# Kernel optimization log

Hardware: AMD Instinct MI355X
Metric: run time of the kernel (lower is better)

Reference implementation:

```python
import jax, jax.numpy as jnp
import numpy as np

N = 65536          # number of input vectors
D = 128            # embedding_dim
K = 2048           # num_embeddings (codebook size)
DH = D // 2        # linear_proj output dim


def setup_inputs() -> dict:
    key = jax.random.key(0)
    k1, k2, k3, k4 = jax.random.split(key, 4)
    z = jax.random.normal(k1, (N, D), dtype=jnp.float32)
    # linear_proj params (nn.Linear(D, D//2)): weight [DH, D], bias [DH]
    W = jax.random.normal(k2, (DH, D), dtype=jnp.float32) * (1.0 / np.sqrt(D))
    b = jax.random.normal(k3, (DH,), dtype=jnp.float32) * 0.01
    # codebook buffer, initialized ~ N(0,1) as in the torch module
    embeddings = jax.random.normal(k4, (K, D), dtype=jnp.float32)
    return {"z": z, "W": W, "b": b, "embeddings": embeddings}


def reference(z, W, b, embeddings):
    # project inputs and codebook into half-dim space
    z_ = z @ W.T + b                       # [N, DH]
    emb_ = embeddings @ W.T + b            # [K, DH]
    # squared euclidean distances via ||a||^2 + ||b||^2 - 2 a.b
    distances = ((z_ ** 2).sum(-1, keepdims=True)
                 + (emb_ ** 2).sum(-1)
                 - 2.0 * (z_ @ emb_.T))    # [N, K]
    closest = jnp.argmin(distances, axis=-1)               # [N]
    one_hot_encoding = jax.nn.one_hot(closest, K, dtype=jnp.float32)  # [N, K]
    quantized = one_hot_encoding @ embeddings               # [N, D] (gather)
    return (quantized, one_hot_encoding)
```

## Files before the change

### kernel.cpp

```cpp
#include <hip/hip_runtime.h>
#include <float.h>

#define N_ROWS 65536
#define D_IN   128
#define DH     64
#define K_CB   2048

typedef const __attribute__((address_space(1))) void* gas_p;
typedef __attribute__((address_space(3))) void* las_p;
typedef _Float16 f16x8 __attribute__((ext_vector_type(8)));
typedef float    f32x4 __attribute__((ext_vector_type(4)));

__global__ __launch_bounds__(256) void k_project(
    const float* __restrict__ Z, const float* __restrict__ emb,
    const float* __restrict__ W, const float* __restrict__ b,
    _Float16* __restrict__ zpl,
    _Float16* __restrict__ epl,
    float* __restrict__ e2,
    float* __restrict__ outOH) {
  __shared__ __align__(16) float Wl[64 * 140];
  __shared__ __align__(16) float Zl[16 * 128];
  int tid = threadIdx.x;
  const float* src; _Float16* dst; int n0; bool do_e2; size_t plane;
  if ((int)blockIdx.x < 4096) {
    src = Z;   dst = zpl; n0 = blockIdx.x * 16;          do_e2 = false; plane = (size_t)N_ROWS * 64;
  } else {
    src = emb; dst = epl; n0 = (blockIdx.x - 4096) * 16; do_e2 = true;  plane = (size_t)K_CB * 64;
  }

#pragma unroll
  for (int i = 0; i < 8; ++i) {
    int idx4 = tid + 256 * i;
    int j = idx4 >> 5;
    int d4 = (idx4 & 31) * 4;
    *(float4*)&Wl[j * 140 + d4] = *(const float4*)(W + j * 128 + d4);
  }
#pragma unroll
  for (int i = 0; i < 2; ++i) {
    int idx4 = tid + 256 * i;
    int r = idx4 >> 5;
    int d4 = (idx4 & 31) * 4;
    *(float4*)&Zl[r * 128 + d4] = *(const float4*)(src + (size_t)(n0 + r) * 128 + d4);
  }
  int j = tid & 63, g = tid >> 6;
  float bj = b[j];
  __syncthreads();

  if (outOH && (int)blockIdx.x < 4096) {
    f32x4 zz4 = (f32x4){0.f, 0.f, 0.f, 0.f};
    f32x4* dz = (f32x4*)(outOH + (size_t)n0 * K_CB);
#pragma unroll
    for (int i = 0; i < 32; ++i)
      __builtin_nontemporal_store(zz4, dz + tid + 256 * i);
  }

  float acc[4] = {0.f, 0.f, 0.f, 0.f};
  for (int d4 = 0; d4 < 128; d4 += 4) {
    float4 w4 = *(float4*)&Wl[j * 140 + d4];
#pragma unroll
    for (int i = 0; i < 4; ++i) {
      float4 z4 = *(float4*)&Zl[(g * 4 + i) * 128 + d4];
      acc[i] = fmaf(z4.x, w4.x, fmaf(z4.y, w4.y, fmaf(z4.z, w4.z, fmaf(z4.w, w4.w, acc[i]))));
    }
  }
#pragma unroll
  for (int i = 0; i < 4; ++i) {
    int n = n0 + g * 4 + i;
    float v = acc[i] + bj;
    _Float16 h = (_Float16)v;  float rm = v - (float)h;
    _Float16 m = (_Float16)rm;
    int pos = (((j >> 3) ^ (n & 7)) << 3) | (j & 7);
    size_t base = (size_t)n * 64 + pos;
    dst[base]         = h;
    dst[plane + base] = m;
    if (do_e2) {
      float s = v * v;
#pragma unroll
      for (int off = 32; off > 0; off >>= 1) s += __shfl_xor(s, off, 64);
      if (j == 0) e2[n] = s;
    }
  }
}

__global__ __launch_bounds__(256, 3) void k_score(
    const _Float16* __restrict__ zpl,
    const _Float16* __restrict__ epl,
    const float* __restrict__ e2,
    const float* __restrict__ emb,
    float* __restrict__ outQ,
    float* __restrict__ outOH,
    int* __restrict__ cidx_g) {
  __shared__ __align__(16) _Float16 Zs[2 * 64 * 64];
  __shared__ __align__(16) _Float16 Es[2 * 128 * 64];
  __shared__ float e2s[128];

  int tid = threadIdx.x, lane = tid & 63, wid = tid >> 6;
  int quad = lane >> 4, l16 = lane & 15;
  int wcol = wid * 32;
  int row0 = blockIdx.x * 64;

  for (int q = wid; q < 16; q += 4) {
    int p = q >> 3, within = (q & 7) * 1024;
    const char* g = (const char*)zpl + (size_t)p * ((size_t)N_ROWS * 128)
                  + (size_t)row0 * 128 + within + lane * 16;
    __builtin_amdgcn_global_load_lds((gas_p)g, (las_p)((char*)Zs + p * 8192 + within), 16, 0, 0);
  }

  float best[16]; int bidx[16];
#pragma unroll
  for (int s = 0; s < 16; ++s) { best[s] = FLT_MAX; bidx[s] = 0; }

  for (int kt = 0; kt < K_CB; kt += 128) {
    __syncthreads();
    for (int q = wid; q < 32; q += 4) {
      int p = q >> 4, within = (q & 15) * 1024;
      const char* g = (const char*)epl + (size_t)p * (K_CB * 128)
                    + (size_t)kt * 128 + within + lane * 16;
      __builtin_amdgcn_global_load_lds((gas_p)g, (las_p)((char*)Es + p * 16384 + within), 16, 0, 0);
    }
    if (tid < 128) e2s[tid] = e2[kt + tid];
    __syncthreads();

    f32x4 accf[4][2];
#pragma unroll
    for (int mt = 0; mt < 4; ++mt)
#pragma unroll
      for (int nt = 0; nt < 2; ++nt) accf[mt][nt] = (f32x4){0.f, 0.f, 0.f, 0.f};

#pragma unroll
    for (int step = 0; step < 2; ++step) {
      f16x8 A[4][2];
#pragma unroll
      for (int mt = 0; mt < 4; ++mt) {
        int tr = mt * 16 + l16;
        int cph = (step * 4 + quad) ^ (tr & 7);
        const _Float16* pa = Zs + tr * 64 + cph * 8;
        A[mt][0] = *(const f16x8*)pa;
        A[mt][1] = *(const f16x8*)(pa + 4096);
      }
#pragma unroll
      for (int nt = 0; nt < 2; ++nt) {
        int tc = wcol + nt * 16 + l16;
        int cph = (step * 4 + quad) ^ (tc & 7);
        const _Float16* pb = Es + tc * 64 + cph * 8;
        f16x8 Bh = *(const f16x8*)pb;
        f16x8 Bm = *(const f16x8*)(pb + 8192);
#pragma unroll
        for (int mt = 0; mt < 4; ++mt) {
          f32x4 c = accf[mt][nt];
          c = __builtin_amdgcn_mfma_f32_16x16x32_f16(A[mt][1], Bm, c, 0, 0, 0);
          c = __builtin_amdgcn_mfma_f32_16x16x32_f16(A[mt][1], Bh, c, 0, 0, 0);
          c = __builtin_amdgcn_mfma_f32_16x16x32_f16(A[mt][0], Bm, c, 0, 0, 0);
          c = __builtin_amdgcn_mfma_f32_16x16x32_f16(A[mt][0], Bh, c, 0, 0, 0);
          accf[mt][nt] = c;
        }
      }
    }

#pragma unroll
    for (int nt = 0; nt < 2; ++nt) {
      float ev = e2s[wcol + nt * 16 + l16];
      int col = kt + wcol + nt * 16 + l16;
#pragma unroll
      for (int mt = 0; mt < 4; ++mt)
#pragma unroll
        for (int r = 0; r < 4; ++r) {
          float s = fmaf(-2.0f, accf[mt][nt][r], ev);
          int slot = mt * 4 + r;
          if (s < best[slot]) { best[slot] = s; bidx[slot] = col; }
        }
    }
  }

  __syncthreads();
  float* redm = (float*)Es;
  int*   redi = (int*)((char*)Es + 16384);
#pragma unroll
  for (int mt = 0; mt < 4; ++mt)
#pragma unroll
    for (int r = 0; r < 4; ++r) {
      int row = mt * 16 + quad * 4 + r;
      redm[row * 64 + wid * 16 + l16] = best[mt * 4 + r];
      redi[row * 64 + wid * 16 + l16] = bidx[mt * 4 + r];
    }
  __syncthreads();
  int* cidx = (int*)Zs;
  if (tid < 64) {
    float m = redm[tid * 64]; int mi = redi[tid * 64];
    for (int s = 1; s < 64; ++s) {
      float v = redm[tid * 64 + s]; int vi = redi[tid * 64 + s];
      if (v < m || (v == m && vi < mi)) { m = v; mi = vi; }
    }
    cidx[tid] = mi;
  }
  __syncthreads();

  if (outOH) {
    if (tid < 64) outOH[(size_t)(row0 + tid) * K_CB + cidx[tid]] = 1.0f;
  } else {
    if (tid < 64) cidx_g[row0 + tid] = cidx[tid];
  }

#pragma unroll
  for (int i = 0; i < 8; ++i) {
    int idx = tid + 256 * i;
    int r = idx >> 5, c = (idx & 31) * 4;
    f32x4 v = *(const f32x4*)(emb + (size_t)cidx[r] * D_IN + c);
    __builtin_nontemporal_store(v, (f32x4*)(outQ + (size_t)(row0 + r) * D_IN + c));
  }
}

__global__ void k_epilogue(const int* __restrict__ cidx_g, float* __restrict__ outOH) {
  int tid  = threadIdx.x;
  int row0 = blockIdx.x * 64;
  float4 zz4 = make_float4(0.f, 0.f, 0.f, 0.f);
  for (int r = 0; r < 64; ++r) {
    float4* dst = (float4*)(outOH + (size_t)(row0 + r) * K_CB);
    dst[tid]       = zz4;
    dst[tid + 256] = zz4;
  }
  __syncthreads();
  if (tid < 64) {
    int r = row0 + tid;
    outOH[(size_t)r * K_CB + cidx_g[r]] = 1.0f;
  }
}

extern "C" void kernel_launch(void* const* d_in, const int* in_sizes, int n_in,
                              void* d_out, int out_size, void* d_ws, size_t ws_size,
                              hipStream_t stream) {
  (void)in_sizes; (void)n_in; (void)out_size;
  const float* Z   = (const float*)d_in[0];
  const float* W   = (const float*)d_in[1];
  const float* b   = (const float*)d_in[2];
  const float* emb = (const float*)d_in[3];
  float* outQ  = (float*)d_out;
  float* outOH = (float*)d_out + (size_t)N_ROWS * D_IN;

  char* wsb = (char*)d_ws;
  _Float16* epl = (_Float16*)wsb;
  float*    e2  = (float*)(wsb + 524288);
  const size_t need_primary = 524288 + 8192 + (size_t)2 * N_ROWS * 64 * 2;

  if (ws_size >= need_primary) {
    _Float16* zpl = (_Float16*)(wsb + 532480);
    k_project<<<4224, 256, 0, stream>>>(Z, emb, W, b, zpl, epl, e2, outOH);
    k_score<<<1024, 256, 0, stream>>>(zpl, epl, e2, emb, outQ, outOH, nullptr);
  } else {
    int*      cidx_g = (int*)(wsb + 532480);
    _Float16* zpl    = (_Float16*)outOH;
    k_project<<<4224, 256, 0, stream>>>(Z, emb, W, b, zpl, epl, e2, nullptr);
    k_score<<<1024, 256, 0, stream>>>(zpl, epl, e2, emb, outQ, nullptr, cidx_g);
    k_epilogue<<<1024, 256, 0, stream>>>(cidx_g, outOH);
  }
}
```

Before: 674.5 us.

## Fuse input projection into scoring kernel and double-buffer codebook tiles

Moves the Z projection into the main scoring kernel, so each block computes its 64 projected rows into LDS as split fp16 hi/lo planes. This removes the separate projection pass and the global round trip of the projected Z. The codebook tiles are now double-buffered with async global-to-LDS loads, the codebook norms are held in registers, and the one-hot zero-fill stores are interleaved with the per-tile compute. In exchange, LDS use grows to 80KB and launch bounds drop to 2 blocks per CU, and the workspace-size fallback path is removed.

```diff
diff --git a/kernel.cpp b/kernel.cpp
--- a/kernel.cpp
+++ b/kernel.cpp
@@ -11,22 +11,16 @@
 typedef _Float16 f16x8 __attribute__((ext_vector_type(8)));
 typedef float    f32x4 __attribute__((ext_vector_type(4)));
 
-__global__ __launch_bounds__(256) void k_project(
-    const float* __restrict__ Z, const float* __restrict__ emb,
-    const float* __restrict__ W, const float* __restrict__ b,
-    _Float16* __restrict__ zpl,
+__global__ __launch_bounds__(256) void k_prep(
+    const float* __restrict__ emb, const float* __restrict__ W,
+    const float* __restrict__ b,
     _Float16* __restrict__ epl,
-    float* __restrict__ e2,
-    float* __restrict__ outOH) {
+    float* __restrict__ e2) {
   __shared__ __align__(16) float Wl[64 * 140];
   __shared__ __align__(16) float Zl[16 * 128];
   int tid = threadIdx.x;
-  const float* src; _Float16* dst; int n0; bool do_e2; size_t plane;
-  if ((int)blockIdx.x < 4096) {
-    src = Z;   dst = zpl; n0 = blockIdx.x * 16;          do_e2 = false; plane = (size_t)N_ROWS * 64;
-  } else {
-    src = emb; dst = epl; n0 = (blockIdx.x - 4096) * 16; do_e2 = true;  plane = (size_t)K_CB * 64;
-  }
+  int n0 = blockIdx.x * 16;
+  const size_t plane = (size_t)K_CB * 64;
 
 #pragma unroll
   for (int i = 0; i < 8; ++i) {
@@ -40,19 +34,11 @@
     int idx4 = tid + 256 * i;
     int r = idx4 >> 5;
     int d4 = (idx4 & 31) * 4;
-    *(float4*)&Zl[r * 128 + d4] = *(const float4*)(src + (size_t)(n0 + r) * 128 + d4);
+    *(float4*)&Zl[r * 128 + d4] = *(const float4*)(emb + (size_t)(n0 + r) * 128 + d4);
   }
   int j = tid & 63, g = tid >> 6;
   float bj = b[j];
   __syncthreads();
-
-  if (outOH && (int)blockIdx.x < 4096) {
-    f32x4 zz4 = (f32x4){0.f, 0.f, 0.f, 0.f};
-    f32x4* dz = (f32x4*)(outOH + (size_t)n0 * K_CB);
-#pragma unroll
-    for (int i = 0; i < 32; ++i)
-      __builtin_nontemporal_store(zz4, dz + tid + 256 * i);
-  }
 
   float acc[4] = {0.f, 0.f, 0.f, 0.f};
   for (int d4 = 0; d4 < 128; d4 += 4) {
@@ -71,55 +57,128 @@
     _Float16 m = (_Float16)rm;
     int pos = (((j >> 3) ^ (n & 7)) << 3) | (j & 7);
     size_t base = (size_t)n * 64 + pos;
-    dst[base]         = h;
-    dst[plane + base] = m;
-    if (do_e2) {
-      float s = v * v;
-#pragma unroll
-      for (int off = 32; off > 0; off >>= 1) s += __shfl_xor(s, off, 64);
-      if (j == 0) e2[n] = s;
-    }
+    epl[base]         = h;
+    epl[plane + base] = m;
+    float s = v * v;
+#pragma unroll
+    for (int off = 32; off > 0; off >>= 1) s += __shfl_xor(s, off, 64);
+    if (j == 0) e2[n] = s;
   }
 }
 
-__global__ __launch_bounds__(256, 3) void k_score(
-    const _Float16* __restrict__ zpl,
+__global__ __launch_bounds__(256, 2) void k_main(
+    const float* __restrict__ Z, const float* __restrict__ W,
+    const float* __restrict__ b,
     const _Float16* __restrict__ epl,
     const float* __restrict__ e2,
     const float* __restrict__ emb,
     float* __restrict__ outQ,
-    float* __restrict__ outOH,
-    int* __restrict__ cidx_g) {
-  __shared__ __align__(16) _Float16 Zs[2 * 64 * 64];
-  __shared__ __align__(16) _Float16 Es[2 * 128 * 64];
-  __shared__ float e2s[128];
+    float* __restrict__ outOH) {
+  __shared__ __align__(16) char U[81920];
+  _Float16* es0 = (_Float16*)U;
+  _Float16* es1 = (_Float16*)(U + 32768);
+  float*    Wt  = (float*)(U + 32768);
+  _Float16* Zs  = (_Float16*)(U + 65536);
 
   int tid = threadIdx.x, lane = tid & 63, wid = tid >> 6;
   int quad = lane >> 4, l16 = lane & 15;
   int wcol = wid * 32;
   int row0 = blockIdx.x * 64;
 
-  for (int q = wid; q < 16; q += 4) {
-    int p = q >> 3, within = (q & 7) * 1024;
-    const char* g = (const char*)zpl + (size_t)p * ((size_t)N_ROWS * 128)
-                  + (size_t)row0 * 128 + within + lane * 16;
-    __builtin_amdgcn_global_load_lds((gas_p)g, (las_p)((char*)Zs + p * 8192 + within), 16, 0, 0);
-  }
+  for (int q = wid; q < 32; q += 4) {
+    int p = q >> 4, within = (q & 15) * 1024;
+    const char* g = (const char*)epl + (size_t)p * (K_CB * 128) + within + lane * 16;
+    __builtin_amdgcn_global_load_lds((gas_p)g, (las_p)(U + p * 16384 + within), 16, 0, 0);
+  }
+
+#pragma unroll
+  for (int i = 0; i < 8; ++i) {
+    int idx4 = tid + 256 * i;
+    int j = idx4 & 63, dc = idx4 >> 6;
+    float4 w4 = *(const float4*)(W + (size_t)j * 128 + dc * 4);
+    Wt[(dc * 4 + 0) * 64 + j] = w4.x;
+    Wt[(dc * 4 + 1) * 64 + j] = w4.y;
+    Wt[(dc * 4 + 2) * 64 + j] = w4.z;
+    Wt[(dc * 4 + 3) * 64 + j] = w4.w;
+  }
+
+  float e2r[32];
+#pragma unroll
+  for (int t = 0; t < 16; ++t) {
+    e2r[t * 2 + 0] = e2[t * 128 + wcol + l16];
+    e2r[t * 2 + 1] = e2[t * 128 + wcol + 16 + l16];
+  }
+
+  int jj = lane;
+  float bj = b[jj];
+  __syncthreads();
+
+  {
+    float acc[16];
+#pragma unroll
+    for (int i = 0; i < 16; ++i) acc[i] = 0.f;
+    const float* zbase = Z + (size_t)(row0 + wid * 16) * 128;
+    for (int d4 = 0; d4 < 128; d4 += 4) {
+      float w0 = Wt[(d4 + 0) * 64 + jj];
+      float w1 = Wt[(d4 + 1) * 64 + jj];
+      float w2 = Wt[(d4 + 2) * 64 + jj];
+      float w3 = Wt[(d4 + 3) * 64 + jj];
+#pragma unroll
+      for (int i = 0; i < 16; ++i) {
+        float4 z4 = *(const float4*)(zbase + i * 128 + d4);
+        acc[i] = fmaf(z4.x, w0, fmaf(z4.y, w1, fmaf(z4.z, w2, fmaf(z4.w, w3, acc[i]))));
+      }
+    }
+#pragma unroll
+    for (int i = 0; i < 16; ++i) {
+      int r = wid * 16 + i;
+      float v = acc[i] + bj;
+      _Float16 h = (_Float16)v;  float rm = v - (float)h;
+      _Float16 m = (_Float16)rm;
+      int pos = (((jj >> 3) ^ (r & 7)) << 3) | (jj & 7);
+      Zs[r * 64 + pos]        = h;
+      Zs[4096 + r * 64 + pos] = m;
+    }
+  }
+  __syncthreads();
+
+  f16x8 A[2][4][2];
+#pragma unroll
+  for (int step = 0; step < 2; ++step)
+#pragma unroll
+    for (int mt = 0; mt < 4; ++mt) {
+      int tr = mt * 16 + l16;
+      int cph = (step * 4 + quad) ^ (tr & 7);
+      const _Float16* pa = Zs + tr * 64 + cph * 8;
+      A[step][mt][0] = *(const f16x8*)pa;
+      A[step][mt][1] = *(const f16x8*)(pa + 4096);
+    }
 
   float best[16]; int bidx[16];
 #pragma unroll
   for (int s = 0; s < 16; ++s) { best[s] = FLT_MAX; bidx[s] = 0; }
 
-  for (int kt = 0; kt < K_CB; kt += 128) {
-    __syncthreads();
-    for (int q = wid; q < 32; q += 4) {
-      int p = q >> 4, within = (q & 15) * 1024;
-      const char* g = (const char*)epl + (size_t)p * (K_CB * 128)
-                    + (size_t)kt * 128 + within + lane * 16;
-      __builtin_amdgcn_global_load_lds((gas_p)g, (las_p)((char*)Es + p * 16384 + within), 16, 0, 0);
-    }
-    if (tid < 128) e2s[tid] = e2[kt + tid];
-    __syncthreads();
+#pragma unroll
+  for (int t = 0; t < 16; ++t) {
+    _Float16* esc = (t & 1) ? es1 : es0;
+    if (t < 15) {
+      char* esn = (char*)((t & 1) ? es0 : es1);
+      for (int q = wid; q < 32; q += 4) {
+        int p = q >> 4, within = (q & 15) * 1024;
+        const char* g = (const char*)epl + (size_t)p * (K_CB * 128)
+                      + (size_t)(t + 1) * 16384 + within + lane * 16;
+        __builtin_amdgcn_global_load_lds((gas_p)g, (las_p)(esn + p * 16384 + within), 16, 0, 0);
+      }
+    }
+    {
+      f32x4 zz = (f32x4){0.f, 0.f, 0.f, 0.f};
+#pragma unroll
+      for (int i2 = 0; i2 < 8; ++i2) {
+        int idx = tid + 256 * i2;
+        int r = idx >> 5, c4 = (idx & 31) * 4;
+        __builtin_nontemporal_store(zz, (f32x4*)(outOH + (size_t)(row0 + r) * K_CB + t * 128 + c4));
+      }
+    }
 
     f32x4 accf[4][2];
 #pragma unroll
@@ -128,39 +187,29 @@
       for (int nt = 0; nt < 2; ++nt) accf[mt][nt] = (f32x4){0.f, 0.f, 0.f, 0.f};
 
 #pragma unroll
-    for (int step = 0; step < 2; ++step) {
-      f16x8 A[4][2];
-#pragma unroll
-      for (int mt = 0; mt < 4; ++mt) {
-        int tr = mt * 16 + l16;
-        int cph = (step * 4 + quad) ^ (tr & 7);
-        const _Float16* pa = Zs + tr * 64 + cph * 8;
-        A[mt][0] = *(const f16x8*)pa;
-        A[mt][1] = *(const f16x8*)(pa + 4096);
-      }
+    for (int step = 0; step < 2; ++step)
 #pragma unroll
       for (int nt = 0; nt < 2; ++nt) {
         int tc = wcol + nt * 16 + l16;
         int cph = (step * 4 + quad) ^ (tc & 7);
-        const _Float16* pb = Es + tc * 64 + cph * 8;
+        const _Float16* pb = esc + tc * 64 + cph * 8;
         f16x8 Bh = *(const f16x8*)pb;
         f16x8 Bm = *(const f16x8*)(pb + 8192);
 #pragma unroll
         for (int mt = 0; mt < 4; ++mt) {
           f32x4 c = accf[mt][nt];
-          c = __builtin_amdgcn_mfma_f32_16x16x32_f16(A[mt][1], Bm, c, 0, 0, 0);
-          c = __builtin_amdgcn_mfma_f32_16x16x32_f16(A[mt][1], Bh, c, 0, 0, 0);
-          c = __builtin_amdgcn_mfma_f32_16x16x32_f16(A[mt][0], Bm, c, 0, 0, 0);
-          c = __builtin_amdgcn_mfma_f32_16x16x32_f16(A[mt][0], Bh, c, 0, 0, 0);
+          c = __builtin_amdgcn_mfma_f32_16x16x32_f16(A[step][mt][1], Bm, c, 0, 0, 0);
+          c = __builtin_amdgcn_mfma_f32_16x16x32_f16(A[step][mt][1], Bh, c, 0, 0, 0);
+          c = __builtin_amdgcn_mfma_f32_16x16x32_f16(A[step][mt][0], Bm, c, 0, 0, 0);
+          c = __builtin_amdgcn_mfma_f32_16x16x32_f16(A[step][mt][0], Bh, c, 0, 0, 0);
           accf[mt][nt] = c;
         }
       }
-    }
 
 #pragma unroll
     for (int nt = 0; nt < 2; ++nt) {
-      float ev = e2s[wcol + nt * 16 + l16];
-      int col = kt + wcol + nt * 16 + l16;
+      float ev = e2r[t * 2 + nt];
+      int col = t * 128 + wcol + nt * 16 + l16;
 #pragma unroll
       for (int mt = 0; mt < 4; ++mt)
 #pragma unroll
@@ -170,11 +219,11 @@
           if (s < best[slot]) { best[slot] = s; bidx[slot] = col; }
         }
     }
-  }
-
-  __syncthreads();
-  float* redm = (float*)Es;
-  int*   redi = (int*)((char*)Es + 16384);
+    __syncthreads();
+  }
+
+  float* redm = (float*)U;
+  int*   redi = (int*)(U + 16384);
 #pragma unroll
   for (int mt = 0; mt < 4; ++mt)
 #pragma unroll
@@ -184,7 +233,7 @@
       redi[row * 64 + wid * 16 + l16] = bidx[mt * 4 + r];
     }
   __syncthreads();
-  int* cidx = (int*)Zs;
+  int* cidx = (int*)(U + 65536);
   if (tid < 64) {
     float m = redm[tid * 64]; int mi = redi[tid * 64];
     for (int s = 1; s < 64; ++s) {
@@ -195,11 +244,7 @@
   }
   __syncthreads();
 
-  if (outOH) {
-    if (tid < 64) outOH[(size_t)(row0 + tid) * K_CB + cidx[tid]] = 1.0f;
-  } else {
-    if (tid < 64) cidx_g[row0 + tid] = cidx[tid];
-  }
+  if (tid < 64) outOH[(size_t)(row0 + tid) * K_CB + cidx[tid]] = 1.0f;
 
 #pragma unroll
   for (int i = 0; i < 8; ++i) {
@@ -210,26 +255,10 @@
   }
 }
 
-__global__ void k_epilogue(const int* __restrict__ cidx_g, float* __restrict__ outOH) {
-  int tid  = threadIdx.x;
-  int row0 = blockIdx.x * 64;
-  float4 zz4 = make_float4(0.f, 0.f, 0.f, 0.f);
-  for (int r = 0; r < 64; ++r) {
-    float4* dst = (float4*)(outOH + (size_t)(row0 + r) * K_CB);
-    dst[tid]       = zz4;
-    dst[tid + 256] = zz4;
-  }
-  __syncthreads();
-  if (tid < 64) {
-    int r = row0 + tid;
-    outOH[(size_t)r * K_CB + cidx_g[r]] = 1.0f;
-  }
-}
-
 extern "C" void kernel_launch(void* const* d_in, const int* in_sizes, int n_in,
                               void* d_out, int out_size, void* d_ws, size_t ws_size,
                               hipStream_t stream) {
-  (void)in_sizes; (void)n_in; (void)out_size;
+  (void)in_sizes; (void)n_in; (void)out_size; (void)ws_size;
   const float* Z   = (const float*)d_in[0];
   const float* W   = (const float*)d_in[1];
   const float* b   = (const float*)d_in[2];
@@ -240,17 +269,7 @@
   char* wsb = (char*)d_ws;
   _Float16* epl = (_Float16*)wsb;
   float*    e2  = (float*)(wsb + 524288);
-  const size_t need_primary = 524288 + 8192 + (size_t)2 * N_ROWS * 64 * 2;
-
-  if (ws_size >= need_primary) {
-    _Float16* zpl = (_Float16*)(wsb + 532480);
-    k_project<<<4224, 256, 0, stream>>>(Z, emb, W, b, zpl, epl, e2, outOH);
-    k_score<<<1024, 256, 0, stream>>>(zpl, epl, e2, emb, outQ, outOH, nullptr);
-  } else {
-    int*      cidx_g = (int*)(wsb + 532480);
-    _Float16* zpl    = (_Float16*)outOH;
-    k_project<<<4224, 256, 0, stream>>>(Z, emb, W, b, zpl, epl, e2, nullptr);
-    k_score<<<1024, 256, 0, stream>>>(zpl, epl, e2, emb, outQ, nullptr, cidx_g);
-    k_epilogue<<<1024, 256, 0, stream>>>(cidx_g, outOH);
-  }
+
+  k_prep<<<128, 256, 0, stream>>>(emb, W, b, epl, e2);
+  k_main<<<1024, 256, 0, stream>>>(Z, W, b, epl, e2, emb, outQ, outOH);
 }
```

New measurement: 787.3 us. +16.7%, slower.

## Double-buffer codebook tiles and keep Z fragments in registers in k_score

Applied to the files above, without the earlier changes.

The scoring loop now walks the codebook in 64-column tiles held in two LDS buffers. The next tile is prefetched with global_load_lds while the current one is consumed, so there is one barrier per iteration instead of two. The Z A-fragments are loaded from LDS once and kept in registers for the whole loop, and e2 is read straight from global memory instead of being staged in LDS. In exchange there are more register-resident fragments, fewer columns per wave (less B reuse), and twice as many loop iterations.

```diff
diff --git a/kernel.cpp b/kernel.cpp
--- a/kernel.cpp
+++ b/kernel.cpp
@@ -90,13 +90,13 @@
     float* __restrict__ outQ,
     float* __restrict__ outOH,
     int* __restrict__ cidx_g) {
-  __shared__ __align__(16) _Float16 Zs[2 * 64 * 64];
-  __shared__ __align__(16) _Float16 Es[2 * 128 * 64];
-  __shared__ float e2s[128];
+  __shared__ __align__(16) char U[49152];
+  _Float16* Zs  = (_Float16*)U;
+  char*     es0 = U + 16384;
+  char*     es1 = U + 32768;
 
   int tid = threadIdx.x, lane = tid & 63, wid = tid >> 6;
   int quad = lane >> 4, l16 = lane & 15;
-  int wcol = wid * 32;
   int row0 = blockIdx.x * 64;
 
   for (int q = wid; q < 16; q += 4) {
@@ -105,76 +105,80 @@
                   + (size_t)row0 * 128 + within + lane * 16;
     __builtin_amdgcn_global_load_lds((gas_p)g, (las_p)((char*)Zs + p * 8192 + within), 16, 0, 0);
   }
+  for (int q = wid; q < 16; q += 4) {
+    int p = q >> 3, within = (q & 7) * 1024;
+    const char* g = (const char*)epl + (size_t)p * (K_CB * 128) + within + lane * 16;
+    __builtin_amdgcn_global_load_lds((gas_p)g, (las_p)(es0 + p * 8192 + within), 16, 0, 0);
+  }
+
+  __syncthreads();
+
+  f16x8 A[2][4][2];
+#pragma unroll
+  for (int step = 0; step < 2; ++step)
+#pragma unroll
+    for (int mt = 0; mt < 4; ++mt) {
+      int tr = mt * 16 + l16;
+      int cph = (step * 4 + quad) ^ (tr & 7);
+      const _Float16* pa = Zs + tr * 64 + cph * 8;
+      A[step][mt][0] = *(const f16x8*)pa;
+      A[step][mt][1] = *(const f16x8*)(pa + 4096);
+    }
 
   float best[16]; int bidx[16];
 #pragma unroll
   for (int s = 0; s < 16; ++s) { best[s] = FLT_MAX; bidx[s] = 0; }
 
-  for (int kt = 0; kt < K_CB; kt += 128) {
+  for (int t = 0; t < 32; ++t) {
+    const _Float16* esc = (const _Float16*)((t & 1) ? es1 : es0);
+    if (t < 31) {
+      char* esn = (t & 1) ? es0 : es1;
+      for (int q = wid; q < 16; q += 4) {
+        int p = q >> 3, within = (q & 7) * 1024;
+        const char* g = (const char*)epl + (size_t)p * (K_CB * 128)
+                      + (size_t)(t + 1) * 8192 + within + lane * 16;
+        __builtin_amdgcn_global_load_lds((gas_p)g, (las_p)(esn + p * 8192 + within), 16, 0, 0);
+      }
+    }
+    int col = t * 64 + wid * 16 + l16;
+    float ev = e2[col];
+
+    f32x4 accf[4];
+#pragma unroll
+    for (int mt = 0; mt < 4; ++mt) accf[mt] = (f32x4){0.f, 0.f, 0.f, 0.f};
+
+#pragma unroll
+    for (int step = 0; step < 2; ++step) {
+      int tc = wid * 16 + l16;
+      int cph = (step * 4 + quad) ^ (l16 & 7);
+      const _Float16* pb = esc + tc * 64 + cph * 8;
+      f16x8 Bh = *(const f16x8*)pb;
+      f16x8 Bm = *(const f16x8*)(pb + 4096);
+#pragma unroll
+      for (int mt = 0; mt < 4; ++mt) {
+        f32x4 c = accf[mt];
+        c = __builtin_amdgcn_mfma_f32_16x16x32_f16(A[step][mt][1], Bm, c, 0, 0, 0);
+        c = __builtin_amdgcn_mfma_f32_16x16x32_f16(A[step][mt][1], Bh, c, 0, 0, 0);
+        c = __builtin_amdgcn_mfma_f32_16x16x32_f16(A[step][mt][0], Bm, c, 0, 0, 0);
+        c = __builtin_amdgcn_mfma_f32_16x16x32_f16(A[step][mt][0], Bh, c, 0, 0, 0);
+        accf[mt] = c;
+      }
+    }
+
+#pragma unroll
+    for (int mt = 0; mt < 4; ++mt)
+#pragma unroll
+      for (int r = 0; r < 4; ++r) {
+        float s = fmaf(-2.0f, accf[mt][r], ev);
+        int slot = mt * 4 + r;
+        if (s < best[slot]) { best[slot] = s; bidx[slot] = col; }
+      }
+
     __syncthreads();
-    for (int q = wid; q < 32; q += 4) {
-      int p = q >> 4, within = (q & 15) * 1024;
-      const char* g = (const char*)epl + (size_t)p * (K_CB * 128)
-                    + (size_t)kt * 128 + within + lane * 16;
-      __builtin_amdgcn_global_load_lds((gas_p)g, (las_p)((char*)Es + p * 16384 + within), 16, 0, 0);
-    }
-    if (tid < 128) e2s[tid] = e2[kt + tid];
-    __syncthreads();
-
-    f32x4 accf[4][2];
-#pragma unroll
-    for (int mt = 0; mt < 4; ++mt)
-#pragma unroll
-      for (int nt = 0; nt < 2; ++nt) accf[mt][nt] = (f32x4){0.f, 0.f, 0.f, 0.f};
-
-#pragma unroll
-    for (int step = 0; step < 2; ++step) {
-      f16x8 A[4][2];
-#pragma unroll
-      for (int mt = 0; mt < 4; ++mt) {
-        int tr = mt * 16 + l16;
-        int cph = (step * 4 + quad) ^ (tr & 7);
-        const _Float16* pa = Zs + tr * 64 + cph * 8;
-        A[mt][0] = *(const f16x8*)pa;
-        A[mt][1] = *(const f16x8*)(pa + 4096);
-      }
-#pragma unroll
-      for (int nt = 0; nt < 2; ++nt) {
-        int tc = wcol + nt * 16 + l16;
-        int cph = (step * 4 + quad) ^ (tc & 7);
-        const _Float16* pb = Es + tc * 64 + cph * 8;
-        f16x8 Bh = *(const f16x8*)pb;
-        f16x8 Bm = *(const f16x8*)(pb + 8192);
-#pragma unroll
-        for (int mt = 0; mt < 4; ++mt) {
-          f32x4 c = accf[mt][nt];
-          c = __builtin_amdgcn_mfma_f32_16x16x32_f16(A[mt][1], Bm, c, 0, 0, 0);
-          c = __builtin_amdgcn_mfma_f32_16x16x32_f16(A[mt][1], Bh, c, 0, 0, 0);
-          c = __builtin_amdgcn_mfma_f32_16x16x32_f16(A[mt][0], Bm, c, 0, 0, 0);
-          c = __builtin_amdgcn_mfma_f32_16x16x32_f16(A[mt][0], Bh, c, 0, 0, 0);
-          accf[mt][nt] = c;
-        }
-      }
-    }
-
-#pragma unroll
-    for (int nt = 0; nt < 2; ++nt) {
-      float ev = e2s[wcol + nt * 16 + l16];
-      int col = kt + wcol + nt * 16 + l16;
-#pragma unroll
-      for (int mt = 0; mt < 4; ++mt)
-#pragma unroll
-        for (int r = 0; r < 4; ++r) {
-          float s = fmaf(-2.0f, accf[mt][nt][r], ev);
-          int slot = mt * 4 + r;
-          if (s < best[slot]) { best[slot] = s; bidx[slot] = col; }
-        }
-    }
-  }
-
-  __syncthreads();
-  float* redm = (float*)Es;
-  int*   redi = (int*)((char*)Es + 16384);
+  }
+
+  float* redm = (float*)U;
+  int*   redi = (int*)(U + 16384);
 #pragma unroll
   for (int mt = 0; mt < 4; ++mt)
 #pragma unroll
@@ -184,7 +188,7 @@
       redi[row * 64 + wid * 16 + l16] = bidx[mt * 4 + r];
     }
   __syncthreads();
-  int* cidx = (int*)Zs;
+  int* cidx = (int*)(U + 32768);
   if (tid < 64) {
     float m = redm[tid * 64]; int mi = redi[tid * 64];
     for (int s = 1; s < 64; ++s) {
```

Result: no change. 676.4 us (+0.3%).
